# Kernel optimization log

Hardware: AMD Instinct MI355X
Metric: run time of the kernel (lower is better)

The kernel has to match this reference:

```python
import jax, jax.numpy as jnp
import numpy as np


def setup_inputs() -> dict:
    key = jax.random.key(0)
    ks = jax.random.split(key, 9)
    C_in, C_out, D = 64, 64, 24
    B, H, W = 4, 96, 96
    s_in = 1.0 / np.sqrt(C_in)
    s_d = 1.0 / np.sqrt(D)
    return {
        "x": jax.random.normal(ks[0], (B, C_in, H, W), dtype=jnp.float32),
        "wq": jax.random.uniform(ks[1], (D, C_in), jnp.float32, -s_in, s_in),
        "bq": jax.random.uniform(ks[2], (D,), jnp.float32, -s_in, s_in),
        "wk": jax.random.uniform(ks[3], (D, C_in), jnp.float32, -s_in, s_in),
        "bk": jax.random.uniform(ks[4], (D,), jnp.float32, -s_in, s_in),
        "wv": jax.random.uniform(ks[5], (D, C_in), jnp.float32, -s_in, s_in),
        "bv": jax.random.uniform(ks[6], (D,), jnp.float32, -s_in, s_in),
        "wo": jax.random.uniform(ks[7], (C_out, D), jnp.float32, -s_d, s_d),
        "bo": jax.random.uniform(ks[8], (C_out,), jnp.float32, -s_d, s_d),
    }


def reference(x, wq, bq, wk, bk, wv, bv, wo, bo):
    B, C, H, W = x.shape
    D = wq.shape[0]
    xf = x.reshape(B, C, H * W)  # [B, C, N]
    # 1x1 convs == channel-wise linear projections
    q = jnp.einsum('dc,bcn->bdn', wq, xf) + bq[None, :, None]  # [B, D, N]
    k = jnp.einsum('dc,bcn->bdn', wk, xf) + bk[None, :, None]
    v = jnp.einsum('dc,bcn->bdn', wv, xf) + bv[None, :, None]
    scale = 1.0 / jnp.sqrt(jnp.asarray(D, x.dtype))
    scores = jnp.einsum('bdi,bdj->bij', q, k) * scale  # [B, N, N]
    weights = jax.nn.softmax(scores, axis=-1)
    # attn_out[b,d,i] = sum_j v[b,d,j] * weights[b,i,j]
    attn = jnp.einsum('bdj,bij->bdi', v, weights)  # [B, D, N]
    out = jnp.einsum('od,bdn->bon', wo, attn) + bo[None, :, None]
    return out.reshape(B, -1, H, W)
```

## Files before the change

kernel.cpp:

```cpp
#include <hip/hip_runtime.h>
#include <stdint.h>

#define NPIX 9216
#define CIN 64
#define DD 24
#define DP 32
#define JQ 1152
#define NIT 18

typedef __attribute__((ext_vector_type(8))) short short8;
typedef __attribute__((ext_vector_type(4))) float f32x4;
typedef __attribute__((ext_vector_type(4))) unsigned int u32x4;

__device__ __forceinline__ unsigned short f2bf(float f) {
    unsigned int u = __builtin_bit_cast(unsigned int, f);
    u += 0x7fffu + ((u >> 16) & 1u);
    return (unsigned short)(u >> 16);
}
__device__ __forceinline__ unsigned int pkbf(float lo, float hi) {
    unsigned int r;
    asm("v_cvt_pk_bf16_f32 %0, %1, %2" : "=v"(r) : "v"(lo), "v"(hi));
    return r;
}

__global__ __launch_bounds__(256) void qkv_proj_kernel(
    const float* __restrict__ x,
    const float* __restrict__ wq, const float* __restrict__ bq,
    const float* __restrict__ wk, const float* __restrict__ bk,
    const float* __restrict__ wv, const float* __restrict__ bv,
    unsigned short* __restrict__ qr, unsigned short* __restrict__ kr,
    unsigned short* __restrict__ vdn)
{
    const int p = blockIdx.y;
    const int tid = blockIdx.x * 256 + threadIdx.x;
    const int b = tid / NPIX;
    const int n = tid - b * NPIX;
    const float* xb = x + (size_t)b * CIN * NPIX + n;
    float xv[CIN];
#pragma unroll
    for (int c = 0; c < CIN; ++c) xv[c] = xb[(size_t)c * NPIX];

    const float* wm = (p == 0) ? wq : (p == 1) ? wk : wv;
    const float* bm = (p == 0) ? bq : (p == 1) ? bk : bv;

    float acc[DD];
#pragma unroll
    for (int d = 0; d < DD; ++d) acc[d] = bm[d];
#pragma unroll 4
    for (int c = 0; c < CIN; ++c) {
        const float xc = xv[c];
#pragma unroll
        for (int d = 0; d < DD; ++d) acc[d] = fmaf(wm[d * CIN + c], xc, acc[d]);
    }

    if (p == 2) {
        const size_t vbase = (size_t)b * DD * NPIX + n;
#pragma unroll
        for (int d = 0; d < DD; ++d) vdn[vbase + (size_t)d * NPIX] = f2bf(acc[d]);
    } else {
        alignas(16) unsigned short row[DP];
        const float sc = (p == 0) ? (float)(0.20412414523193154 * 1.4426950408889634) : 1.0f;
#pragma unroll
        for (int d = 0; d < DD; ++d) row[d] = f2bf(acc[d] * sc);
#pragma unroll
        for (int d = DD; d < DP; ++d) row[d] = 0;
        unsigned short* dst = ((p == 0) ? qr : kr) + (size_t)(b * NPIX + n) * DP;
        const u32x4* r4 = (const u32x4*)row;
#pragma unroll
        for (int i = 0; i < 4; ++i) ((u32x4*)dst)[i] = r4[i];
    }
}

__global__ __launch_bounds__(256) void attn_kernel(
    const unsigned short* __restrict__ qr,
    const unsigned short* __restrict__ kr,
    const unsigned short* __restrict__ vdn,
    float* __restrict__ part)
{
    __shared__ __align__(16) unsigned char pool[20480 + 18432];
    unsigned short* kpool = (unsigned short*)pool;
    unsigned short* vpool = (unsigned short*)(pool + 20480);

    const int tile = blockIdx.x, jh = blockIdx.y, b = blockIdx.z;
    const int t = threadIdx.x;
    const int w = t >> 6, lane = t & 63;
    const int g = lane >> 4, c = lane & 15;
    const int p = w;

    for (int i = t; i < 4 * 8 * 72; i += 256) {
        const int q_ = i / 576, rem = i - q_ * 576;
        const int r_ = rem / 72, col = rem - r_ * 72;
        vpool[q_ * 2304 + (24 + r_) * 72 + col] = (r_ == 0) ? (unsigned short)0x3F80 : 0;
    }

    const int qbase = tile * 64 + c;
    const unsigned short* qp = qr + (size_t)b * NPIX * DP;
    const short8 qfA = *(const short8*)(qp + (size_t)(qbase +  0) * DP + g * 8);
    const short8 qfB = *(const short8*)(qp + (size_t)(qbase + 16) * DP + g * 8);
    const short8 qfC = *(const short8*)(qp + (size_t)(qbase + 32) * DP + g * 8);
    const short8 qfD = *(const short8*)(qp + (size_t)(qbase + 48) * DP + g * 8);

    const unsigned short* kb = kr + (size_t)b * NPIX * DP;
    const unsigned short* vb = vdn + (size_t)b * DD * NPIX;
    const int jbase = jh * 4608;

    const int kjn = (t >> 1) & 63, khw = t & 1, kqa = t >> 7;
    const int kR = ((kjn >> 5) & 1) * 32 + ((kjn >> 2) & 1) * 16
                 + ((kjn >> 4) & 1) * 8 + ((kjn >> 3) & 1) * 4 + (kjn & 3);
    unsigned short* kdst0 = kpool + kqa * 2560 + kR * 40 + khw * 16;
    unsigned short* kdst1 = kdst0 + 2 * 2560;
    const unsigned short* ksrcA = kb + ((size_t)(jbase + kqa * JQ + kjn)) * DP + khw * 16;
    const unsigned short* ksrcB = ksrcA + (size_t)2 * JQ * DP;

    const int g0 = t, g1 = t + 256, g2 = t + 512;
    const int vq0 = g0 / 192, vr0 = g0 - vq0 * 192, vd0 = vr0 >> 3, vp0 = vr0 & 7;
    const int vq1 = g1 / 192, vr1 = g1 - vq1 * 192, vd1 = vr1 >> 3, vp1 = vr1 & 7;
    const int vq2 = g2 / 192, vr2 = g2 - vq2 * 192, vd2 = vr2 >> 3, vp2 = vr2 & 7;
    unsigned short* vdst0 = vpool + vq0 * 2304 + vd0 * 72 + vp0 * 8;
    unsigned short* vdst1 = vpool + vq1 * 2304 + vd1 * 72 + vp1 * 8;
    unsigned short* vdst2 = vpool + vq2 * 2304 + vd2 * 72 + vp2 * 8;
    const unsigned short* vsrcA = vb + (size_t)vd0 * NPIX + jbase + vq0 * JQ + vp0 * 8;
    const unsigned short* vsrcB = vb + (size_t)vd1 * NPIX + jbase + vq1 * JQ + vp1 * 8;
    const unsigned short* vsrcC = vb + (size_t)vd2 * NPIX + jbase + vq2 * JQ + vp2 * 8;

    const unsigned short* kT = kpool + p * 2560;
    const unsigned short* vT = vpool + p * 2304;

    f32x4 aA0 = {0.f,0.f,0.f,0.f}, aA1 = aA0;
    f32x4 aB0 = aA0, aB1 = aA0;
    f32x4 aC0 = aA0, aC1 = aA0;
    f32x4 aD0 = aA0, aD1 = aA0;
    const f32x4 zf = {0.f, 0.f, 0.f, 0.f};

    u32x4 pk0a, pk0b, pk1a, pk1b, pv0, pv1, pv2;
    {
        const u32x4* s0 = (const u32x4*)ksrcA; pk0a = s0[0]; pk0b = s0[1];
        const u32x4* s1 = (const u32x4*)ksrcB; pk1a = s1[0]; pk1b = s1[1];
        pv0 = *(const u32x4*)vsrcA; pv1 = *(const u32x4*)vsrcB; pv2 = *(const u32x4*)vsrcC;
    }

    for (int it = 0; it < NIT; ++it) {
        __syncthreads();
        *(u32x4*)kdst0 = pk0a; *(u32x4*)(kdst0 + 8) = pk0b;
        *(u32x4*)kdst1 = pk1a; *(u32x4*)(kdst1 + 8) = pk1b;
        *(u32x4*)vdst0 = pv0; *(u32x4*)vdst1 = pv1; *(u32x4*)vdst2 = pv2;
        __syncthreads();

        if (it + 1 < NIT) {
            const int jn = (it + 1) * 64;
            const u32x4* s0 = (const u32x4*)(ksrcA + (size_t)jn * DP); pk0a = s0[0]; pk0b = s0[1];
            const u32x4* s1 = (const u32x4*)(ksrcB + (size_t)jn * DP); pk1a = s1[0]; pk1b = s1[1];
            pv0 = *(const u32x4*)(vsrcA + jn);
            pv1 = *(const u32x4*)(vsrcB + jn);
            pv2 = *(const u32x4*)(vsrcC + jn);
        }

        const short8 kf0 = *(const short8*)(kT + ( 0 + c) * 40 + g * 8);
        const short8 kf1 = *(const short8*)(kT + (16 + c) * 40 + g * 8);
        const short8 kf2 = *(const short8*)(kT + (32 + c) * 40 + g * 8);
        const short8 kf3 = *(const short8*)(kT + (48 + c) * 40 + g * 8);
        const short8 vl0 = *(const short8*)(vT + (c)      * 72 +      g * 8);
        const short8 vh0 = *(const short8*)(vT + (16 + c) * 72 +      g * 8);
        const short8 vl1 = *(const short8*)(vT + (c)      * 72 + 32 + g * 8);
        const short8 vh1 = *(const short8*)(vT + (16 + c) * 72 + 32 + g * 8);

        {
            __builtin_amdgcn_s_setprio(1);
            f32x4 sA0 = __builtin_amdgcn_mfma_f32_16x16x32_bf16(kf0, qfA, zf, 0, 0, 0);
            f32x4 sA1 = __builtin_amdgcn_mfma_f32_16x16x32_bf16(kf1, qfA, zf, 0, 0, 0);
            f32x4 sA2 = __builtin_amdgcn_mfma_f32_16x16x32_bf16(kf2, qfA, zf, 0, 0, 0);
            f32x4 sA3 = __builtin_amdgcn_mfma_f32_16x16x32_bf16(kf3, qfA, zf, 0, 0, 0);
            f32x4 sB0 = __builtin_amdgcn_mfma_f32_16x16x32_bf16(kf0, qfB, zf, 0, 0, 0);
            f32x4 sB1 = __builtin_amdgcn_mfma_f32_16x16x32_bf16(kf1, qfB, zf, 0, 0, 0);
            f32x4 sB2 = __builtin_amdgcn_mfma_f32_16x16x32_bf16(kf2, qfB, zf, 0, 0, 0);
            f32x4 sB3 = __builtin_amdgcn_mfma_f32_16x16x32_bf16(kf3, qfB, zf, 0, 0, 0);
            __builtin_amdgcn_s_setprio(0);

            union { short8 s8; unsigned int u32[4]; } fa0, fa1, fb0, fb1;
            {
                float p0[4], p1[4], p2[4], p3[4];
#pragma unroll
                for (int r = 0; r < 4; ++r) {
                    p0[r] = __builtin_amdgcn_exp2f(sA0[r]);
                    p1[r] = __builtin_amdgcn_exp2f(sA1[r]);
                    p2[r] = __builtin_amdgcn_exp2f(sA2[r]);
                    p3[r] = __builtin_amdgcn_exp2f(sA3[r]);
                }
                fa0.u32[0] = pkbf(p0[0], p0[1]); fa0.u32[1] = pkbf(p0[2], p0[3]);
                fa0.u32[2] = pkbf(p1[0], p1[1]); fa0.u32[3] = pkbf(p1[2], p1[3]);
                fa1.u32[0] = pkbf(p2[0], p2[1]); fa1.u32[1] = pkbf(p2[2], p2[3]);
                fa1.u32[2] = pkbf(p3[0], p3[1]); fa1.u32[3] = pkbf(p3[2], p3[3]);
            }
            {
                float p0[4], p1[4], p2[4], p3[4];
#pragma unroll
                for (int r = 0; r < 4; ++r) {
                    p0[r] = __builtin_amdgcn_exp2f(sB0[r]);
                    p1[r] = __builtin_amdgcn_exp2f(sB1[r]);
                    p2[r] = __builtin_amdgcn_exp2f(sB2[r]);
                    p3[r] = __builtin_amdgcn_exp2f(sB3[r]);
                }
                fb0.u32[0] = pkbf(p0[0], p0[1]); fb0.u32[1] = pkbf(p0[2], p0[3]);
                fb0.u32[2] = pkbf(p1[0], p1[1]); fb0.u32[3] = pkbf(p1[2], p1[3]);
                fb1.u32[0] = pkbf(p2[0], p2[1]); fb1.u32[1] = pkbf(p2[2], p2[3]);
                fb1.u32[2] = pkbf(p3[0], p3[1]); fb1.u32[3] = pkbf(p3[2], p3[3]);
            }

            __builtin_amdgcn_s_setprio(1);
            aA0 = __builtin_amdgcn_mfma_f32_16x16x32_bf16(vl0, fa0.s8, aA0, 0, 0, 0);
            aA1 = __builtin_amdgcn_mfma_f32_16x16x32_bf16(vh0, fa0.s8, aA1, 0, 0, 0);
            aA0 = __builtin_amdgcn_mfma_f32_16x16x32_bf16(vl1, fa1.s8, aA0, 0, 0, 0);
            aA1 = __builtin_amdgcn_mfma_f32_16x16x32_bf16(vh1, fa1.s8, aA1, 0, 0, 0);
            aB0 = __builtin_amdgcn_mfma_f32_16x16x32_bf16(vl0, fb0.s8, aB0, 0, 0, 0);
            aB1 = __builtin_amdgcn_mfma_f32_16x16x32_bf16(vh0, fb0.s8, aB1, 0, 0, 0);
            aB0 = __builtin_amdgcn_mfma_f32_16x16x32_bf16(vl1, fb1.s8, aB0, 0, 0, 0);
            aB1 = __builtin_amdgcn_mfma_f32_16x16x32_bf16(vh1, fb1.s8, aB1, 0, 0, 0);
            __builtin_amdgcn_s_setprio(0);
        }
        {
            __builtin_amdgcn_s_setprio(1);
            f32x4 sC0 = __builtin_amdgcn_mfma_f32_16x16x32_bf16(kf0, qfC, zf, 0, 0, 0);
            f32x4 sC1 = __builtin_amdgcn_mfma_f32_16x16x32_bf16(kf1, qfC, zf, 0, 0, 0);
            f32x4 sC2 = __builtin_amdgcn_mfma_f32_16x16x32_bf16(kf2, qfC, zf, 0, 0, 0);
            f32x4 sC3 = __builtin_amdgcn_mfma_f32_16x16x32_bf16(kf3, qfC, zf, 0, 0, 0);
            f32x4 sD0 = __builtin_amdgcn_mfma_f32_16x16x32_bf16(kf0, qfD, zf, 0, 0, 0);
            f32x4 sD1 = __builtin_amdgcn_mfma_f32_16x16x32_bf16(kf1, qfD, zf, 0, 0, 0);
            f32x4 sD2 = __builtin_amdgcn_mfma_f32_16x16x32_bf16(kf2, qfD, zf, 0, 0, 0);
            f32x4 sD3 = __builtin_amdgcn_mfma_f32_16x16x32_bf16(kf3, qfD, zf, 0, 0, 0);
            __builtin_amdgcn_s_setprio(0);

            union { short8 s8; unsigned int u32[4]; } fc0, fc1, fd0, fd1;
            {
                float p0[4], p1[4], p2[4], p3[4];
#pragma unroll
                for (int r = 0; r < 4; ++r) {
                    p0[r] = __builtin_amdgcn_exp2f(sC0[r]);
                    p1[r] = __builtin_amdgcn_exp2f(sC1[r]);
                    p2[r] = __builtin_amdgcn_exp2f(sC2[r]);
                    p3[r] = __builtin_amdgcn_exp2f(sC3[r]);
                }
                fc0.u32[0] = pkbf(p0[0], p0[1]); fc0.u32[1] = pkbf(p0[2], p0[3]);
                fc0.u32[2] = pkbf(p1[0], p1[1]); fc0.u32[3] = pkbf(p1[2], p1[3]);
                fc1.u32[0] = pkbf(p2[0], p2[1]); fc1.u32[1] = pkbf(p2[2], p2[3]);
                fc1.u32[2] = pkbf(p3[0], p3[1]); fc1.u32[3] = pkbf(p3[2], p3[3]);
            }
            {
                float p0[4], p1[4], p2[4], p3[4];
#pragma unroll
                for (int r = 0; r < 4; ++r) {
                    p0[r] = __builtin_amdgcn_exp2f(sD0[r]);
                    p1[r] = __builtin_amdgcn_exp2f(sD1[r]);
                    p2[r] = __builtin_amdgcn_exp2f(sD2[r]);
                    p3[r] = __builtin_amdgcn_exp2f(sD3[r]);
                }
                fd0.u32[0] = pkbf(p0[0], p0[1]); fd0.u32[1] = pkbf(p0[2], p0[3]);
                fd0.u32[2] = pkbf(p1[0], p1[1]); fd0.u32[3] = pkbf(p1[2], p1[3]);
                fd1.u32[0] = pkbf(p2[0], p2[1]); fd1.u32[1] = pkbf(p2[2], p2[3]);
                fd1.u32[2] = pkbf(p3[0], p3[1]); fd1.u32[3] = pkbf(p3[2], p3[3]);
            }

            __builtin_amdgcn_s_setprio(1);
            aC0 = __builtin_amdgcn_mfma_f32_16x16x32_bf16(vl0, fc0.s8, aC0, 0, 0, 0);
            aC1 = __builtin_amdgcn_mfma_f32_16x16x32_bf16(vh0, fc0.s8, aC1, 0, 0, 0);
            aC0 = __builtin_amdgcn_mfma_f32_16x16x32_bf16(vl1, fc1.s8, aC0, 0, 0, 0);
            aC1 = __builtin_amdgcn_mfma_f32_16x16x32_bf16(vh1, fc1.s8, aC1, 0, 0, 0);
            aD0 = __builtin_amdgcn_mfma_f32_16x16x32_bf16(vl0, fd0.s8, aD0, 0, 0, 0);
            aD1 = __builtin_amdgcn_mfma_f32_16x16x32_bf16(vh0, fd0.s8, aD1, 0, 0, 0);
            aD0 = __builtin_amdgcn_mfma_f32_16x16x32_bf16(vl1, fd1.s8, aD0, 0, 0, 0);
            aD1 = __builtin_amdgcn_mfma_f32_16x16x32_bf16(vh1, fd1.s8, aD1, 0, 0, 0);
            __builtin_amdgcn_s_setprio(0);
        }
    }
    __syncthreads();

    float* om = (float*)pool;
    *(f32x4*)(om + (p * 64 + c)      * 36 + 4 * g) = aA0;
    *(f32x4*)(om + (p * 64 + c)      * 36 + 16 + 4 * g) = aA1;
    *(f32x4*)(om + (p * 64 + 16 + c) * 36 + 4 * g) = aB0;
    *(f32x4*)(om + (p * 64 + 16 + c) * 36 + 16 + 4 * g) = aB1;
    *(f32x4*)(om + (p * 64 + 32 + c) * 36 + 4 * g) = aC0;
    *(f32x4*)(om + (p * 64 + 32 + c) * 36 + 16 + 4 * g) = aC1;
    *(f32x4*)(om + (p * 64 + 48 + c) * 36 + 4 * g) = aD0;
    *(f32x4*)(om + (p * 64 + 48 + c) * 36 + 16 + 4 * g) = aD1;
    __syncthreads();

    const int q = t & 63, og = t >> 6;
    const float* o0 = om + (0 * 64 + q) * 36;
    const float* o1 = om + (1 * 64 + q) * 36;
    const float* o2 = om + (2 * 64 + q) * 36;
    const float* o3 = om + (3 * 64 + q) * 36;
    float* dst = part + ((size_t)((b * 2 + jh) * NPIX + tile * 64 + q)) * 26;
#pragma unroll
    for (int k = 0; k < 7; ++k) {
        const int i = og * 7 + k;
        if (i < 25) dst[i] = (o0[i] + o1[i]) + (o2[i] + o3[i]);
    }
}

__global__ __launch_bounds__(256) void combine_kernel(
    const float* __restrict__ part,
    const float* __restrict__ wo, const float* __restrict__ bo,
    float* __restrict__ out)
{
    __shared__ float od_lds[64][25];
    __shared__ float wo_lds[64 * DD];
    __shared__ float bo_lds[64];
    const int tile = blockIdx.x, b = blockIdx.y;
    const int t = threadIdx.x;
    for (int i = t; i < 64 * DD; i += 256) wo_lds[i] = wo[i];
    if (t < 64) bo_lds[t] = bo[t];

    const int q = t & 63, c2 = t >> 6;
    {
        const float* pA = part + ((size_t)((b * 2 + 0) * NPIX + tile * 64 + q)) * 26;
        const float* pB = part + ((size_t)((b * 2 + 1) * NPIX + tile * 64 + q)) * 26;
#pragma unroll
        for (int k = 0; k < 7; ++k) {
            const int i = c2 * 7 + k;
            if (i < 25) od_lds[q][i] = pA[i] + pB[i];
        }
    }
    __syncthreads();

    const float inv = 1.0f / od_lds[q][24];
    float od[DD];
#pragma unroll
    for (int d = 0; d < DD; ++d) od[d] = od_lds[q][d] * inv;

    const int n_g = tile * 64 + q;
#pragma unroll
    for (int oo = 0; oo < 16; ++oo) {
        const int o = c2 * 16 + oo;
        float a = bo_lds[o];
#pragma unroll
        for (int d = 0; d < DD; ++d) a = fmaf(wo_lds[o * DD + d], od[d], a);
        out[((size_t)(b * 64 + o)) * NPIX + n_g] = a;
    }
}

extern "C" void kernel_launch(void* const* d_in, const int* in_sizes, int n_in,
                              void* d_out, int out_size, void* d_ws, size_t ws_size,
                              hipStream_t stream) {
    const float* x  = (const float*)d_in[0];
    const float* wq = (const float*)d_in[1];
    const float* bq = (const float*)d_in[2];
    const float* wk = (const float*)d_in[3];
    const float* bk = (const float*)d_in[4];
    const float* wv = (const float*)d_in[5];
    const float* bv = (const float*)d_in[6];
    const float* wo = (const float*)d_in[7];
    const float* bo = (const float*)d_in[8];
    float* out = (float*)d_out;

    unsigned short* qr  = (unsigned short*)d_ws;
    unsigned short* kr  = qr + (size_t)4 * NPIX * DP;
    unsigned short* vdn = kr + (size_t)4 * NPIX * DP;
    float* part = (float*)((char*)d_ws + 6488064);

    hipLaunchKernelGGL(qkv_proj_kernel, dim3(4 * NPIX / 256, 3), dim3(256), 0, stream,
                       x, wq, bq, wk, bk, wv, bv, qr, kr, vdn);
    hipLaunchKernelGGL(attn_kernel, dim3(NPIX / 64, 2, 4), dim3(256), 0, stream,
                       qr, kr, vdn, part);
    hipLaunchKernelGGL(combine_kernel, dim3(NPIX / 64, 4), dim3(256), 0, stream,
                       part, wo, bo, out);
}
```

Baseline: 117.8 us.

## Load K/V MFMA fragments directly from global memory, drop LDS staging

The attention kernel no longer stages K and V tiles through shared memory with two barriers per iteration. Each wave now reads its MFMA operand fragments straight from global memory, with the K row permutation folded into the addressing. To make this possible, the projection kernel pads V to 32 rows and writes the ones row and zero padding that the kernel used to create in LDS. This removes the barriers and the LDS traffic, at the cost of uncoalesced, redundant global/L2 reads, since the four waves no longer share K/V data through LDS.

Measured after the change: 105.8 us. 10.1% less time.

```diff
diff --git a/kernel.cpp b/kernel.cpp
--- a/kernel.cpp
+++ b/kernel.cpp
@@ -54,9 +54,12 @@
     }
 
     if (p == 2) {
-        const size_t vbase = (size_t)b * DD * NPIX + n;
+        const size_t vbase = (size_t)b * DP * NPIX + n;
 #pragma unroll
         for (int d = 0; d < DD; ++d) vdn[vbase + (size_t)d * NPIX] = f2bf(acc[d]);
+        vdn[vbase + (size_t)24 * NPIX] = (unsigned short)0x3F80;
+#pragma unroll
+        for (int d = 25; d < DP; ++d) vdn[vbase + (size_t)d * NPIX] = 0;
     } else {
         alignas(16) unsigned short row[DP];
         const float sc = (p == 0) ? (float)(0.20412414523193154 * 1.4426950408889634) : 1.0f;
@@ -77,21 +80,13 @@
     const unsigned short* __restrict__ vdn,
     float* __restrict__ part)
 {
-    __shared__ __align__(16) unsigned char pool[20480 + 18432];
-    unsigned short* kpool = (unsigned short*)pool;
-    unsigned short* vpool = (unsigned short*)(pool + 20480);
+    __shared__ float om[4 * 64 * 36];
 
     const int tile = blockIdx.x, jh = blockIdx.y, b = blockIdx.z;
     const int t = threadIdx.x;
     const int w = t >> 6, lane = t & 63;
     const int g = lane >> 4, c = lane & 15;
     const int p = w;
-
-    for (int i = t; i < 4 * 8 * 72; i += 256) {
-        const int q_ = i / 576, rem = i - q_ * 576;
-        const int r_ = rem / 72, col = rem - r_ * 72;
-        vpool[q_ * 2304 + (24 + r_) * 72 + col] = (r_ == 0) ? (unsigned short)0x3F80 : 0;
-    }
 
     const int qbase = tile * 64 + c;
     const unsigned short* qp = qr + (size_t)b * NPIX * DP;
@@ -101,30 +96,13 @@
     const short8 qfD = *(const short8*)(qp + (size_t)(qbase + 48) * DP + g * 8);
 
     const unsigned short* kb = kr + (size_t)b * NPIX * DP;
-    const unsigned short* vb = vdn + (size_t)b * DD * NPIX;
-    const int jbase = jh * 4608;
-
-    const int kjn = (t >> 1) & 63, khw = t & 1, kqa = t >> 7;
-    const int kR = ((kjn >> 5) & 1) * 32 + ((kjn >> 2) & 1) * 16
-                 + ((kjn >> 4) & 1) * 8 + ((kjn >> 3) & 1) * 4 + (kjn & 3);
-    unsigned short* kdst0 = kpool + kqa * 2560 + kR * 40 + khw * 16;
-    unsigned short* kdst1 = kdst0 + 2 * 2560;
-    const unsigned short* ksrcA = kb + ((size_t)(jbase + kqa * JQ + kjn)) * DP + khw * 16;
-    const unsigned short* ksrcB = ksrcA + (size_t)2 * JQ * DP;
-
-    const int g0 = t, g1 = t + 256, g2 = t + 512;
-    const int vq0 = g0 / 192, vr0 = g0 - vq0 * 192, vd0 = vr0 >> 3, vp0 = vr0 & 7;
-    const int vq1 = g1 / 192, vr1 = g1 - vq1 * 192, vd1 = vr1 >> 3, vp1 = vr1 & 7;
-    const int vq2 = g2 / 192, vr2 = g2 - vq2 * 192, vd2 = vr2 >> 3, vp2 = vr2 & 7;
-    unsigned short* vdst0 = vpool + vq0 * 2304 + vd0 * 72 + vp0 * 8;
-    unsigned short* vdst1 = vpool + vq1 * 2304 + vd1 * 72 + vp1 * 8;
-    unsigned short* vdst2 = vpool + vq2 * 2304 + vd2 * 72 + vp2 * 8;
-    const unsigned short* vsrcA = vb + (size_t)vd0 * NPIX + jbase + vq0 * JQ + vp0 * 8;
-    const unsigned short* vsrcB = vb + (size_t)vd1 * NPIX + jbase + vq1 * JQ + vp1 * 8;
-    const unsigned short* vsrcC = vb + (size_t)vd2 * NPIX + jbase + vq2 * JQ + vp2 * 8;
-
-    const unsigned short* kT = kpool + p * 2560;
-    const unsigned short* vT = vpool + p * 2304;
+    const unsigned short* vb = vdn + (size_t)b * DP * NPIX;
+    const int jbase = jh * 4608 + p * JQ;
+
+    const int jinv0 = ((c >> 3) & 1) * 16 + ((c >> 2) & 1) * 8 + (c & 3);
+    const unsigned short* kp = kb + ((size_t)(jbase + jinv0)) * DP + g * 8;
+    const unsigned short* vpl = vb + (size_t)c * NPIX + jbase + g * 8;
+    const unsigned short* vph = vpl + (size_t)16 * NPIX;
 
     f32x4 aA0 = {0.f,0.f,0.f,0.f}, aA1 = aA0;
     f32x4 aB0 = aA0, aB1 = aA0;
@@ -132,37 +110,25 @@
     f32x4 aD0 = aA0, aD1 = aA0;
     const f32x4 zf = {0.f, 0.f, 0.f, 0.f};
 
-    u32x4 pk0a, pk0b, pk1a, pk1b, pv0, pv1, pv2;
-    {
-        const u32x4* s0 = (const u32x4*)ksrcA; pk0a = s0[0]; pk0b = s0[1];
-        const u32x4* s1 = (const u32x4*)ksrcB; pk1a = s1[0]; pk1b = s1[1];
-        pv0 = *(const u32x4*)vsrcA; pv1 = *(const u32x4*)vsrcB; pv2 = *(const u32x4*)vsrcC;
-    }
+    short8 nk0 = *(const short8*)(kp);
+    short8 nk1 = *(const short8*)(kp + 128);
+    short8 nk2 = *(const short8*)(kp + 1024);
+    short8 nk3 = *(const short8*)(kp + 1152);
 
     for (int it = 0; it < NIT; ++it) {
-        __syncthreads();
-        *(u32x4*)kdst0 = pk0a; *(u32x4*)(kdst0 + 8) = pk0b;
-        *(u32x4*)kdst1 = pk1a; *(u32x4*)(kdst1 + 8) = pk1b;
-        *(u32x4*)vdst0 = pv0; *(u32x4*)vdst1 = pv1; *(u32x4*)vdst2 = pv2;
-        __syncthreads();
-
+        const short8 kf0 = nk0, kf1 = nk1, kf2 = nk2, kf3 = nk3;
+        const short8 vl0 = *(const short8*)(vpl);
+        const short8 vh0 = *(const short8*)(vph);
+        const short8 vl1 = *(const short8*)(vpl + 32);
+        const short8 vh1 = *(const short8*)(vph + 32);
+        vpl += 64; vph += 64;
         if (it + 1 < NIT) {
-            const int jn = (it + 1) * 64;
-            const u32x4* s0 = (const u32x4*)(ksrcA + (size_t)jn * DP); pk0a = s0[0]; pk0b = s0[1];
-            const u32x4* s1 = (const u32x4*)(ksrcB + (size_t)jn * DP); pk1a = s1[0]; pk1b = s1[1];
-            pv0 = *(const u32x4*)(vsrcA + jn);
-            pv1 = *(const u32x4*)(vsrcB + jn);
-            pv2 = *(const u32x4*)(vsrcC + jn);
+            kp += 2048;
+            nk0 = *(const short8*)(kp);
+            nk1 = *(const short8*)(kp + 128);
+            nk2 = *(const short8*)(kp + 1024);
+            nk3 = *(const short8*)(kp + 1152);
         }
-
-        const short8 kf0 = *(const short8*)(kT + ( 0 + c) * 40 + g * 8);
-        const short8 kf1 = *(const short8*)(kT + (16 + c) * 40 + g * 8);
-        const short8 kf2 = *(const short8*)(kT + (32 + c) * 40 + g * 8);
-        const short8 kf3 = *(const short8*)(kT + (48 + c) * 40 + g * 8);
-        const short8 vl0 = *(const short8*)(vT + (c)      * 72 +      g * 8);
-        const short8 vh0 = *(const short8*)(vT + (16 + c) * 72 +      g * 8);
-        const short8 vl1 = *(const short8*)(vT + (c)      * 72 + 32 + g * 8);
-        const short8 vh1 = *(const short8*)(vT + (16 + c) * 72 + 32 + g * 8);
 
         {
             __builtin_amdgcn_s_setprio(1);
@@ -271,9 +237,7 @@
             __builtin_amdgcn_s_setprio(0);
         }
     }
-    __syncthreads();
-
-    float* om = (float*)pool;
+
     *(f32x4*)(om + (p * 64 + c)      * 36 + 4 * g) = aA0;
     *(f32x4*)(om + (p * 64 + c)      * 36 + 16 + 4 * g) = aA1;
     *(f32x4*)(om + (p * 64 + 16 + c) * 36 + 4 * g) = aB0;
@@ -355,8 +319,7 @@
     unsigned short* qr  = (unsigned short*)d_ws;
     unsigned short* kr  = qr + (size_t)4 * NPIX * DP;
     unsigned short* vdn = kr + (size_t)4 * NPIX * DP;
-    float* part = (float*)((char*)d_ws + 6488064);
-
+    float* part = (float*)((char*)d_ws + 7077888);
     hipLaunchKernelGGL(qkv_proj_kernel, dim3(4 * NPIX / 256, 3), dim3(256), 0, stream,
                        x, wq, bq, wk, bk, wv, bv, qr, kr, vdn);
     hipLaunchKernelGGL(attn_kernel, dim3(NPIX / 64, 2, 4), dim3(256), 0, stream,
```
